# Kernel optimization log

Hardware: AMD Instinct MI355X
Metric: run time of the kernel (lower is better)

Reference implementation:

```python
import jax, jax.numpy as jnp
import numpy as np

FP8_MAX = 448.0
GROUP_SIZE = 128
AMAX_FLOOR = 1e-4


def setup_inputs() -> dict:
    key = jax.random.key(0)
    M, N = 16384, 4096
    x = jax.random.normal(key, (M, N), dtype=jnp.float32).astype(jnp.bfloat16)
    return {"x": x}


def reference(x):
    # x: [M, N] bf16. Per-token-group dynamic fp8-range quantization.
    M, N = x.shape
    G = GROUP_SIZE
    Ng = N // G
    xf = x.astype(jnp.float32).reshape(M, Ng, G)
    amax = jnp.maximum(jnp.max(jnp.abs(xf), axis=2, keepdims=True), AMAX_FLOOR)
    scale = amax / FP8_MAX                      # [M, Ng, 1]
    y = jnp.clip(xf / scale, -FP8_MAX, FP8_MAX).reshape(M, N)  # fp32 output
    return y, scale.reshape(M, Ng)
```

## Files before the change

kernel.cpp:

```cpp
#include <hip/hip_runtime.h>
#include <hip/hip_bf16.h>


static constexpr float FP8_MAX_F  = 448.0f;
static constexpr float AMAX_FLOOR = 1e-4f;

typedef float floatx4 __attribute__((ext_vector_type(4)));

__device__ __forceinline__ void process_group(const float v[8],
                                              float* __restrict__ y,
                                              float* __restrict__ scale,
                                              long long base, long long gid,
                                              int lane16)
{
    float m = fabsf(v[0]);
#pragma unroll
    for (int i = 1; i < 8; ++i) m = fmaxf(m, fabsf(v[i]));
    m = fmaxf(m, __shfl_xor(m, 1));
    m = fmaxf(m, __shfl_xor(m, 2));
    m = fmaxf(m, __shfl_xor(m, 4));
    m = fmaxf(m, __shfl_xor(m, 8));

    const float amax = fmaxf(m, AMAX_FLOOR);
    const float s    = amax * (1.0f / FP8_MAX_F);
    const float inv  = FP8_MAX_F / amax;

    floatx4 o0, o1;
    o0.x = fminf(fmaxf(v[0] * inv, -FP8_MAX_F), FP8_MAX_F);
    o0.y = fminf(fmaxf(v[1] * inv, -FP8_MAX_F), FP8_MAX_F);
    o0.z = fminf(fmaxf(v[2] * inv, -FP8_MAX_F), FP8_MAX_F);
    o0.w = fminf(fmaxf(v[3] * inv, -FP8_MAX_F), FP8_MAX_F);
    o1.x = fminf(fmaxf(v[4] * inv, -FP8_MAX_F), FP8_MAX_F);
    o1.y = fminf(fmaxf(v[5] * inv, -FP8_MAX_F), FP8_MAX_F);
    o1.z = fminf(fmaxf(v[6] * inv, -FP8_MAX_F), FP8_MAX_F);
    o1.w = fminf(fmaxf(v[7] * inv, -FP8_MAX_F), FP8_MAX_F);

    ((floatx4*)(y + base))[0] = o0;
    ((floatx4*)(y + base))[1] = o1;

    if (lane16 == 0) scale[gid] = s;
}

__device__ __forceinline__ void decode_bf16(const int4 raw, float v[8])
{
    const unsigned int* wp = (const unsigned int*)&raw;
#pragma unroll
    for (int i = 0; i < 4; ++i) {
        const unsigned int w = wp[i];
        v[2 * i]     = __uint_as_float((w & 0xffffu) << 16);
        v[2 * i + 1] = __uint_as_float(w & 0xffff0000u);
    }
}

__global__ __launch_bounds__(256) void quant_v4_kernel(
    const void* __restrict__ xraw,
    float* __restrict__ y,
    float* __restrict__ scale,
    long long n_groups,
    int iters)
{
    __shared__ int flag_s;

    if (threadIdx.x < 64) {
        const unsigned int w  = ((const unsigned int*)xraw)[threadIdx.x];
        const bool lo_nonzero = (w & 0xffffu) != 0u;
        unsigned long long m  = __ballot(lo_nonzero);
        if (threadIdx.x == 0) flag_s = (__popcll(m) >= 32) ? 1 : 0;
    }
    __syncthreads();
    const bool in_bf16 = (flag_s != 0);

    const int lane16 = threadIdx.x & 15;
    const int gsub   = threadIdx.x >> 4;
    const long long tstride = gridDim.x;

    long long tile = blockIdx.x;
    int it = 0;

    if (in_bf16) {
        for (; it + 4 <= iters; it += 4) {
            long long base[4];
            int4 raw[4];
#pragma unroll
            for (int u = 0; u < 4; ++u) {
                const long long gid = (tile + (long long)u * tstride) * 16 + gsub;
                base[u] = gid * 128 + (long long)lane16 * 8;
                raw[u] = *(const int4*)((const __hip_bfloat16*)xraw + base[u]);
            }
#pragma unroll
            for (int u = 0; u < 4; ++u) {
                const long long gid = (tile + (long long)u * tstride) * 16 + gsub;
                float v[8];
                decode_bf16(raw[u], v);
                process_group(v, y, scale, base[u], gid, lane16);
            }
            tile += 4 * tstride;
        }
        for (; it < iters; ++it, tile += tstride) {
            const long long gid  = tile * 16 + gsub;
            const long long base = gid * 128 + (long long)lane16 * 8;
            float v[8];
            decode_bf16(*(const int4*)((const __hip_bfloat16*)xraw + base), v);
            process_group(v, y, scale, base, gid, lane16);
        }
    } else {
        for (; it + 4 <= iters; it += 4) {
            long long base[4];
            floatx4 ra[4], rb[4];
#pragma unroll
            for (int u = 0; u < 4; ++u) {
                const long long gid = (tile + (long long)u * tstride) * 16 + gsub;
                base[u] = gid * 128 + (long long)lane16 * 8;
                ra[u] = ((const floatx4*)((const float*)xraw + base[u]))[0];
                rb[u] = ((const floatx4*)((const float*)xraw + base[u]))[1];
            }
#pragma unroll
            for (int u = 0; u < 4; ++u) {
                const long long gid = (tile + (long long)u * tstride) * 16 + gsub;
                float v[8] = {ra[u].x, ra[u].y, ra[u].z, ra[u].w,
                              rb[u].x, rb[u].y, rb[u].z, rb[u].w};
                process_group(v, y, scale, base[u], gid, lane16);
            }
            tile += 4 * tstride;
        }
        for (; it < iters; ++it, tile += tstride) {
            const long long gid  = tile * 16 + gsub;
            const long long base = gid * 128 + (long long)lane16 * 8;
            const floatx4 a = ((const floatx4*)((const float*)xraw + base))[0];
            const floatx4 b = ((const floatx4*)((const float*)xraw + base))[1];
            float v[8] = {a.x, a.y, a.z, a.w, b.x, b.y, b.z, b.w};
            process_group(v, y, scale, base, gid, lane16);
        }
    }
}

extern "C" void kernel_launch(void* const* d_in, const int* in_sizes, int n_in,
                              void* d_out, int out_size, void* d_ws, size_t ws_size,
                              hipStream_t stream) {
    const long long MN = (long long)in_sizes[0];
    const long long n_groups = MN / 128;

    float* y     = (float*)d_out;
    float* scale = y + MN;

    const int threads = 256;
    const long long tiles = (n_groups + 15) / 16;

    long long blocks = tiles < 2048 ? tiles : 2048;
    while (tiles % blocks != 0) --blocks;
    const int iters = (int)(tiles / blocks);

    quant_v4_kernel<<<(int)blocks, threads, 0, stream>>>(d_in[0], y, scale,
                                                         n_groups, iters);
}
```

Before: 441.8 us.

## Split per-lane group access into two half-group chunks with 32-bit indexing

Measured after the change: 444.0 us. No clear change (+0.5%).

```diff
diff --git a/kernel.cpp b/kernel.cpp
--- a/kernel.cpp
+++ b/kernel.cpp
@@ -7,15 +7,25 @@
 
 typedef float floatx4 __attribute__((ext_vector_type(4)));
 
-__device__ __forceinline__ void process_group(const float v[8],
+__device__ __forceinline__ void decode4(const uint2 w, float v[4])
+{
+    v[0] = __uint_as_float((w.x & 0xffffu) << 16);
+    v[1] = __uint_as_float(w.x & 0xffff0000u);
+    v[2] = __uint_as_float((w.y & 0xffffu) << 16);
+    v[3] = __uint_as_float(w.y & 0xffff0000u);
+}
+
+__device__ __forceinline__ void process_store(const float v[8],
+                                              unsigned e0,
                                               float* __restrict__ y,
                                               float* __restrict__ scale,
-                                              long long base, long long gid,
                                               int lane16)
 {
-    float m = fabsf(v[0]);
-#pragma unroll
-    for (int i = 1; i < 8; ++i) m = fmaxf(m, fabsf(v[i]));
+    float m01 = fmaxf(fabsf(v[0]), fabsf(v[1]));
+    float m23 = fmaxf(fabsf(v[2]), fabsf(v[3]));
+    float m45 = fmaxf(fabsf(v[4]), fabsf(v[5]));
+    float m67 = fmaxf(fabsf(v[6]), fabsf(v[7]));
+    float m = fmaxf(fmaxf(m01, m23), fmaxf(m45, m67));
     m = fmaxf(m, __shfl_xor(m, 1));
     m = fmaxf(m, __shfl_xor(m, 2));
     m = fmaxf(m, __shfl_xor(m, 4));
@@ -23,40 +33,28 @@
 
     const float amax = fmaxf(m, AMAX_FLOOR);
     const float s    = amax * (1.0f / FP8_MAX_F);
-    const float inv  = FP8_MAX_F / amax;
+    const float inv  = FP8_MAX_F * __builtin_amdgcn_rcpf(amax);
 
-    floatx4 o0, o1;
-    o0.x = fminf(fmaxf(v[0] * inv, -FP8_MAX_F), FP8_MAX_F);
-    o0.y = fminf(fmaxf(v[1] * inv, -FP8_MAX_F), FP8_MAX_F);
-    o0.z = fminf(fmaxf(v[2] * inv, -FP8_MAX_F), FP8_MAX_F);
-    o0.w = fminf(fmaxf(v[3] * inv, -FP8_MAX_F), FP8_MAX_F);
-    o1.x = fminf(fmaxf(v[4] * inv, -FP8_MAX_F), FP8_MAX_F);
-    o1.y = fminf(fmaxf(v[5] * inv, -FP8_MAX_F), FP8_MAX_F);
-    o1.z = fminf(fmaxf(v[6] * inv, -FP8_MAX_F), FP8_MAX_F);
-    o1.w = fminf(fmaxf(v[7] * inv, -FP8_MAX_F), FP8_MAX_F);
+    floatx4 oA, oB;
+    oA.x = fminf(fmaxf(v[0] * inv, -FP8_MAX_F), FP8_MAX_F);
+    oA.y = fminf(fmaxf(v[1] * inv, -FP8_MAX_F), FP8_MAX_F);
+    oA.z = fminf(fmaxf(v[2] * inv, -FP8_MAX_F), FP8_MAX_F);
+    oA.w = fminf(fmaxf(v[3] * inv, -FP8_MAX_F), FP8_MAX_F);
+    oB.x = fminf(fmaxf(v[4] * inv, -FP8_MAX_F), FP8_MAX_F);
+    oB.y = fminf(fmaxf(v[5] * inv, -FP8_MAX_F), FP8_MAX_F);
+    oB.z = fminf(fmaxf(v[6] * inv, -FP8_MAX_F), FP8_MAX_F);
+    oB.w = fminf(fmaxf(v[7] * inv, -FP8_MAX_F), FP8_MAX_F);
 
-    ((floatx4*)(y + base))[0] = o0;
-    ((floatx4*)(y + base))[1] = o1;
+    *(floatx4*)(y + e0)       = oA;
+    *(floatx4*)(y + e0 + 64u) = oB;
 
-    if (lane16 == 0) scale[gid] = s;
+    if (lane16 == 0) scale[e0 >> 7] = s;
 }
 
-__device__ __forceinline__ void decode_bf16(const int4 raw, float v[8])
-{
-    const unsigned int* wp = (const unsigned int*)&raw;
-#pragma unroll
-    for (int i = 0; i < 4; ++i) {
-        const unsigned int w = wp[i];
-        v[2 * i]     = __uint_as_float((w & 0xffffu) << 16);
-        v[2 * i + 1] = __uint_as_float(w & 0xffff0000u);
-    }
-}
-
-__global__ __launch_bounds__(256) void quant_v4_kernel(
+__global__ __launch_bounds__(256) void quant_v5_kernel(
     const void* __restrict__ xraw,
     float* __restrict__ y,
     float* __restrict__ scale,
-    long long n_groups,
     int iters)
 {
     __shared__ int flag_s;
@@ -64,72 +62,75 @@
     if (threadIdx.x < 64) {
         const unsigned int w  = ((const unsigned int*)xraw)[threadIdx.x];
         const bool lo_nonzero = (w & 0xffffu) != 0u;
-        unsigned long long m  = __ballot(lo_nonzero);
-        if (threadIdx.x == 0) flag_s = (__popcll(m) >= 32) ? 1 : 0;
+        unsigned long long mm = __ballot(lo_nonzero);
+        if (threadIdx.x == 0) flag_s = (__popcll(mm) >= 32) ? 1 : 0;
     }
     __syncthreads();
     const bool in_bf16 = (flag_s != 0);
 
     const int lane16 = threadIdx.x & 15;
     const int gsub   = threadIdx.x >> 4;
-    const long long tstride = gridDim.x;
+    const unsigned tstride = gridDim.x;
 
-    long long tile = blockIdx.x;
+    unsigned tile = blockIdx.x;
     int it = 0;
 
     if (in_bf16) {
+        const __hip_bfloat16* xb = (const __hip_bfloat16*)xraw;
         for (; it + 4 <= iters; it += 4) {
-            long long base[4];
-            int4 raw[4];
+            unsigned e0[4];
+            uint2 ra[4], rb[4];
 #pragma unroll
             for (int u = 0; u < 4; ++u) {
-                const long long gid = (tile + (long long)u * tstride) * 16 + gsub;
-                base[u] = gid * 128 + (long long)lane16 * 8;
-                raw[u] = *(const int4*)((const __hip_bfloat16*)xraw + base[u]);
+                const unsigned gid = (tile + (unsigned)u * tstride) * 16u + gsub;
+                e0[u] = gid * 128u + (unsigned)lane16 * 4u;
+                ra[u] = *(const uint2*)(xb + e0[u]);
+                rb[u] = *(const uint2*)(xb + e0[u] + 64u);
             }
 #pragma unroll
             for (int u = 0; u < 4; ++u) {
-                const long long gid = (tile + (long long)u * tstride) * 16 + gsub;
                 float v[8];
-                decode_bf16(raw[u], v);
-                process_group(v, y, scale, base[u], gid, lane16);
+                decode4(ra[u], v);
+                decode4(rb[u], v + 4);
+                process_store(v, e0[u], y, scale, lane16);
             }
-            tile += 4 * tstride;
+            tile += 4u * tstride;
         }
         for (; it < iters; ++it, tile += tstride) {
-            const long long gid  = tile * 16 + gsub;
-            const long long base = gid * 128 + (long long)lane16 * 8;
+            const unsigned gid = tile * 16u + gsub;
+            const unsigned e0  = gid * 128u + (unsigned)lane16 * 4u;
             float v[8];
-            decode_bf16(*(const int4*)((const __hip_bfloat16*)xraw + base), v);
-            process_group(v, y, scale, base, gid, lane16);
+            decode4(*(const uint2*)(xb + e0), v);
+            decode4(*(const uint2*)(xb + e0 + 64u), v + 4);
+            process_store(v, e0, y, scale, lane16);
         }
     } else {
+        const float* xf = (const float*)xraw;
         for (; it + 4 <= iters; it += 4) {
-            long long base[4];
+            unsigned e0[4];
             floatx4 ra[4], rb[4];
 #pragma unroll
             for (int u = 0; u < 4; ++u) {
-                const long long gid = (tile + (long long)u * tstride) * 16 + gsub;
-                base[u] = gid * 128 + (long long)lane16 * 8;
-                ra[u] = ((const floatx4*)((const float*)xraw + base[u]))[0];
-                rb[u] = ((const floatx4*)((const float*)xraw + base[u]))[1];
+                const unsigned gid = (tile + (unsigned)u * tstride) * 16u + gsub;
+                e0[u] = gid * 128u + (unsigned)lane16 * 4u;
+                ra[u] = *(const floatx4*)(xf + e0[u]);
+                rb[u] = *(const floatx4*)(xf + e0[u] + 64u);
             }
 #pragma unroll
             for (int u = 0; u < 4; ++u) {
-                const long long gid = (tile + (long long)u * tstride) * 16 + gsub;
                 float v[8] = {ra[u].x, ra[u].y, ra[u].z, ra[u].w,
                               rb[u].x, rb[u].y, rb[u].z, rb[u].w};
-                process_group(v, y, scale, base[u], gid, lane16);
+                process_store(v, e0[u], y, scale, lane16);
             }
-            tile += 4 * tstride;
+            tile += 4u * tstride;
         }
         for (; it < iters; ++it, tile += tstride) {
-            const long long gid  = tile * 16 + gsub;
-            const long long base = gid * 128 + (long long)lane16 * 8;
-            const floatx4 a = ((const floatx4*)((const float*)xraw + base))[0];
-            const floatx4 b = ((const floatx4*)((const float*)xraw + base))[1];
+            const unsigned gid = tile * 16u + gsub;
+            const unsigned e0  = gid * 128u + (unsigned)lane16 * 4u;
+            const floatx4 a = *(const floatx4*)(xf + e0);
+            const floatx4 b = *(const floatx4*)(xf + e0 + 64u);
             float v[8] = {a.x, a.y, a.z, a.w, b.x, b.y, b.z, b.w};
-            process_group(v, y, scale, base, gid, lane16);
+            process_store(v, e0, y, scale, lane16);
         }
     }
 }
@@ -150,6 +151,5 @@
     while (tiles % blocks != 0) --blocks;
     const int iters = (int)(tiles / blocks);
 
-    quant_v4_kernel<<<(int)blocks, threads, 0, stream>>>(d_in[0], y, scale,
-                                                         n_groups, iters);
+    quant_v5_kernel<<<(int)blocks, threads, 0, stream>>>(d_in[0], y, scale, iters);
 }
```
